# Kernel optimization log

Hardware: AMD Instinct MI355X
Metric: run time of the kernel (lower is better)

The kernel has to match this reference:

```python
import jax, jax.numpy as jnp
import numpy as np

H = 128      # num_hidden
HIN = 384    # num_in (h_E feature dim)
DFF = 512    # FFN inner dim = 4*H
SCALE = 30.0
EPS = 1e-5

def gelu(x):
    return jax.nn.gelu(x, approximate=False)

def linear(x, w, b):
    return x @ w.T + b

def layer_norm(x, w, b):
    mu = jnp.mean(x, axis=-1, keepdims=True)
    var = jnp.var(x, axis=-1, keepdims=True)
    return (x - mu) * jax.lax.rsqrt(var + EPS) * w + b


def setup_inputs() -> dict:
    key = jax.random.key(0)
    ks = jax.random.split(key, 10)
    B, N, K = 4, 2048, 48
    s = lambda d: 1.0 / np.sqrt(d)
    return {
        "h_V": jax.random.normal(ks[0], (B, N, H), jnp.float32),
        "h_E": jax.random.normal(ks[1], (B, N, K, HIN), jnp.float32),
        "mask_V": jnp.ones((B, N), jnp.float32),
        "mask_attend": jnp.ones((B, N, K), jnp.float32),
        "W1_w": jax.random.normal(ks[2], (H, H + HIN), jnp.float32) * s(H + HIN),
        "W1_b": jnp.zeros((H,), jnp.float32),
        "W2_w": jax.random.normal(ks[3], (H, H), jnp.float32) * s(H),
        "W2_b": jnp.zeros((H,), jnp.float32),
        "W3_w": jax.random.normal(ks[4], (H, H), jnp.float32) * s(H),
        "W3_b": jnp.zeros((H,), jnp.float32),
        "ln1_w": jnp.ones((H,), jnp.float32),
        "ln1_b": jnp.zeros((H,), jnp.float32),
        "Win_w": jax.random.normal(ks[5], (DFF, H), jnp.float32) * s(H),
        "Win_b": jnp.zeros((DFF,), jnp.float32),
        "Wout_w": jax.random.normal(ks[6], (H, DFF), jnp.float32) * s(DFF),
        "Wout_b": jnp.zeros((H,), jnp.float32),
        "ln2_w": jnp.ones((H,), jnp.float32),
        "ln2_b": jnp.zeros((H,), jnp.float32),
    }


def reference(h_V, h_E, mask_V, mask_attend,
              W1_w, W1_b, W2_w, W2_b, W3_w, W3_b,
              ln1_w, ln1_b, Win_w, Win_b, Wout_w, Wout_b, ln2_w, ln2_b):
    K = h_E.shape[-2]
    # broadcast node feats to neighbors and concat: [B, N, K, H+HIN]
    h_V_expand = jnp.broadcast_to(h_V[:, :, None, :], (*h_V.shape[:2], K, h_V.shape[-1]))
    h_EV = jnp.concatenate([h_V_expand, h_E], axis=-1)
    h_message = linear(gelu(linear(gelu(linear(h_EV, W1_w, W1_b)), W2_w, W2_b)), W3_w, W3_b)
    h_message = mask_attend[..., None] * h_message
    dh = jnp.sum(h_message, axis=-2) / SCALE
    h = layer_norm(h_V + dh, ln1_w, ln1_b)
    dh = linear(gelu(linear(h, Win_w, Win_b)), Wout_w, Wout_b)
    h = layer_norm(h + dh, ln2_w, ln2_b)
    return mask_V[..., None] * h
```

## Files before the change

kernel.cpp:

```cpp
#include <hip/hip_runtime.h>
#include <hip/hip_bf16.h>

#define H    128
#define HIN  384
#define FIN  512
#define KNB  48
#define DFF  512
#define NNODES 8192
#define NNB_F (KNB*HIN)

typedef float f32x4 __attribute__((ext_vector_type(4)));
typedef short bf16x8 __attribute__((ext_vector_type(8)));

__device__ __forceinline__ unsigned short f2bf(float x){
  union { float f; unsigned u; } v; v.f = x;
  unsigned r = v.u + 0x7FFFu + ((v.u >> 16) & 1u);
  return (unsigned short)(r >> 16);
}

__device__ __forceinline__ bf16x8 load8f_bf(const float* p){
  float4 a = *(const float4*)p;
  float4 b = *(const float4*)(p+4);
  bf16x8 o;
  o[0]=(short)f2bf(a.x); o[1]=(short)f2bf(a.y); o[2]=(short)f2bf(a.z); o[3]=(short)f2bf(a.w);
  o[4]=(short)f2bf(b.x); o[5]=(short)f2bf(b.y); o[6]=(short)f2bf(b.z); o[7]=(short)f2bf(b.w);
  return o;
}

__device__ __forceinline__ float gelu_f(float x){
  return 0.5f * x * (1.0f + erff(x * 0.70710678118654752f));
}

__device__ __forceinline__ f32x4 zero4(){ f32x4 z; z[0]=0.f;z[1]=0.f;z[2]=0.f;z[3]=0.f; return z; }

__global__ __launch_bounds__(256) void k_convert(
    const float* __restrict__ W1, const float* __restrict__ W2,
    const float* __restrict__ W3, const float* __restrict__ Win,
    const float* __restrict__ Wout, unsigned short* __restrict__ dst)
{
  int i0 = (blockIdx.x*256 + threadIdx.x)*4;
  #pragma unroll
  for (int t=0;t<4;t++){
    int idx = i0 + t;
    float v;
    if      (idx <  65536) v = W1[idx];
    else if (idx <  81920) v = W2[idx-65536];
    else if (idx <  98304) v = W3[idx-81920];
    else if (idx < 163840) v = Win[idx-98304];
    else                   v = Wout[idx-163840];
    dst[idx] = f2bf(v);
  }
}

__global__ __launch_bounds__(256) void k_bias1(
    const float* __restrict__ hV, const unsigned short* __restrict__ wW1,
    const float* __restrict__ W1b, float* __restrict__ bias1)
{
  int tid = threadIdx.x;
  int wid = tid>>6, lane = tid&63;
  int lr = lane&15, lg = lane>>4;
  int m0 = (blockIdx.x*4 + wid)*16;

  f32x4 acc[8];
  #pragma unroll
  for (int i=0;i<8;i++) acc[i] = zero4();

  #pragma unroll
  for (int ks=0; ks<4; ks++){
    bf16x8 a = load8f_bf(hV + (size_t)(m0+lr)*H + ks*32 + lg*8);
    #pragma unroll
    for (int nt=0; nt<8; nt++){
      bf16x8 b = *(const bf16x8*)(wW1 + (size_t)(nt*16+lr)*FIN + ks*32 + lg*8);
      acc[nt] = __builtin_amdgcn_mfma_f32_16x16x32_bf16(a, b, acc[nt], 0,0,0);
    }
  }
  #pragma unroll
  for (int nt=0; nt<8; nt++){
    int col = nt*16 + lr;
    float bv = W1b[col];
    #pragma unroll
    for (int e=0;e<4;e++){
      int row = lg*4 + e;
      bias1[(size_t)(m0+row)*H + col] = acc[nt][e] + bv;
    }
  }
}

__global__ __launch_bounds__(256) void k_message(
    const float* __restrict__ hV, const float* __restrict__ hE,
    const float* __restrict__ maskA,
    const unsigned short* __restrict__ wW1, const unsigned short* __restrict__ wW2,
    const unsigned short* __restrict__ wW3,
    const float* __restrict__ W2b, const float* __restrict__ W3b,
    const float* __restrict__ ln1w, const float* __restrict__ ln1b,
    const float* __restrict__ bias1, float* __restrict__ hmid)
{
  __shared__ __align__(16) unsigned short sA[48*392];
  __shared__ __align__(16) unsigned short sG1[48*136];
  __shared__ float sMask[48];
  __shared__ float sBias[128];
  __shared__ float sDh[128];

  int node = blockIdx.x;
  int tid  = threadIdx.x;
  const float* hEn = hE + (size_t)node * NNB_F;

  #pragma unroll
  for (int i=0;i<9;i++){
    int c = i*256 + tid;
    int row = c/48, cir = c - row*48;
    bf16x8 v = load8f_bf(hEn + (size_t)c*8);
    *(bf16x8*)(sA + row*392 + cir*8) = v;
  }
  if (tid < 48)  sMask[tid] = maskA[(size_t)node*KNB + tid];
  if (tid < 128) sBias[tid] = bias1[(size_t)node*H + tid];
  __syncthreads();

  int wid = tid>>6, lane = tid&63;
  int lr = lane&15, lg = lane>>4;

  f32x4 acc1[3][2];
  #pragma unroll
  for (int mt=0;mt<3;mt++){ acc1[mt][0]=zero4(); acc1[mt][1]=zero4(); }

  for (int ks=0; ks<12; ks++){
    bf16x8 a[3];
    #pragma unroll
    for (int mt=0;mt<3;mt++)
      a[mt] = *(const bf16x8*)(sA + (mt*16+lr)*392 + ks*32 + lg*8);
    #pragma unroll
    for (int j=0;j<2;j++){
      int nt = wid*2 + j;
      bf16x8 b = *(const bf16x8*)(wW1 + (size_t)(nt*16+lr)*FIN + (H + ks*32 + lg*8));
      #pragma unroll
      for (int mt=0;mt<3;mt++)
        acc1[mt][j] = __builtin_amdgcn_mfma_f32_16x16x32_bf16(a[mt], b, acc1[mt][j], 0,0,0);
    }
  }
  #pragma unroll
  for (int j=0;j<2;j++){
    int col = (wid*2+j)*16 + lr;
    float bv = sBias[col];
    #pragma unroll
    for (int mt=0;mt<3;mt++){
      #pragma unroll
      for (int e=0;e<4;e++){
        float g = gelu_f(acc1[mt][j][e] + bv);
        int row = mt*16 + lg*4 + e;
        sG1[row*136 + col] = f2bf(g);
      }
    }
  }
  __syncthreads();

  f32x4 acc2[3][2];
  #pragma unroll
  for (int mt=0;mt<3;mt++){ acc2[mt][0]=zero4(); acc2[mt][1]=zero4(); }
  #pragma unroll
  for (int ks=0; ks<4; ks++){
    bf16x8 a[3];
    #pragma unroll
    for (int mt=0;mt<3;mt++)
      a[mt] = *(const bf16x8*)(sG1 + (mt*16+lr)*136 + ks*32 + lg*8);
    #pragma unroll
    for (int j=0;j<2;j++){
      int nt = wid*2 + j;
      bf16x8 b = *(const bf16x8*)(wW2 + (size_t)(nt*16+lr)*H + ks*32 + lg*8);
      #pragma unroll
      for (int mt=0;mt<3;mt++)
        acc2[mt][j] = __builtin_amdgcn_mfma_f32_16x16x32_bf16(a[mt], b, acc2[mt][j], 0,0,0);
    }
  }
  unsigned short* sG2 = sA;
  #pragma unroll
  for (int j=0;j<2;j++){
    int col = (wid*2+j)*16 + lr;
    float bv = W2b[col];
    #pragma unroll
    for (int mt=0;mt<3;mt++){
      #pragma unroll
      for (int e=0;e<4;e++){
        float g = gelu_f(acc2[mt][j][e] + bv);
        int row = mt*16 + lg*4 + e;
        sG2[row*136 + col] = f2bf(g);
      }
    }
  }
  __syncthreads();

  f32x4 acc3[3][2];
  #pragma unroll
  for (int mt=0;mt<3;mt++){ acc3[mt][0]=zero4(); acc3[mt][1]=zero4(); }
  #pragma unroll
  for (int ks=0; ks<4; ks++){
    bf16x8 a[3];
    #pragma unroll
    for (int mt=0;mt<3;mt++)
      a[mt] = *(const bf16x8*)(sG2 + (mt*16+lr)*136 + ks*32 + lg*8);
    #pragma unroll
    for (int j=0;j<2;j++){
      int nt = wid*2 + j;
      bf16x8 b = *(const bf16x8*)(wW3 + (size_t)(nt*16+lr)*H + ks*32 + lg*8);
      #pragma unroll
      for (int mt=0;mt<3;mt++)
        acc3[mt][j] = __builtin_amdgcn_mfma_f32_16x16x32_bf16(a[mt], b, acc3[mt][j], 0,0,0);
    }
  }
  #pragma unroll
  for (int j=0;j<2;j++){
    int col = (wid*2+j)*16 + lr;
    float bv = W3b[col];
    float p = 0.f;
    #pragma unroll
    for (int mt=0;mt<3;mt++){
      #pragma unroll
      for (int e=0;e<4;e++){
        int row = mt*16 + lg*4 + e;
        p += (acc3[mt][j][e] + bv) * sMask[row];
      }
    }
    p += __shfl_xor(p, 16);
    p += __shfl_xor(p, 32);
    if (lane < 16) sDh[(wid*2+j)*16 + lane] = p;
  }
  __syncthreads();

  if (wid == 0){
    int c0 = lane, c1 = lane + 64;
    float t0 = hV[(size_t)node*H + c0] + sDh[c0]*(1.0f/30.0f);
    float t1 = hV[(size_t)node*H + c1] + sDh[c1]*(1.0f/30.0f);
    float s = t0 + t1, q = t0*t0 + t1*t1;
    #pragma unroll
    for (int off=1; off<64; off<<=1){ s += __shfl_xor(s, off); q += __shfl_xor(q, off); }
    float mu  = s * (1.0f/128.0f);
    float var = q * (1.0f/128.0f) - mu*mu;
    float rs  = rsqrtf(var + 1e-5f);
    hmid[(size_t)node*H + c0] = (t0-mu)*rs*ln1w[c0] + ln1b[c0];
    hmid[(size_t)node*H + c1] = (t1-mu)*rs*ln1w[c1] + ln1b[c1];
  }
}

__global__ __launch_bounds__(256) void k_ffn(
    const float* __restrict__ hmid, const unsigned short* __restrict__ wWin,
    const unsigned short* __restrict__ wWout,
    const float* __restrict__ Winb, const float* __restrict__ Woutb,
    const float* __restrict__ ln2w, const float* __restrict__ ln2b,
    const float* __restrict__ maskV, float* __restrict__ out)
{
  __shared__ __align__(16) unsigned short sH[32*136];
  __shared__ __align__(16) unsigned short sU[32*520];
  __shared__ float sT[32*132];

  int tid = threadIdx.x;
  int m0 = blockIdx.x * 32;

  #pragma unroll
  for (int i=0;i<2;i++){
    int c = i*256 + tid;
    int row = c>>4, cir = c&15;
    bf16x8 v = load8f_bf(hmid + (size_t)(m0+row)*H + cir*8);
    *(bf16x8*)(sH + row*136 + cir*8) = v;
  }
  __syncthreads();

  int wid = tid>>6, lane = tid&63;
  int lr = lane&15, lg = lane>>4;

  f32x4 acc[2][8];
  #pragma unroll
  for (int mt=0;mt<2;mt++)
    #pragma unroll
    for (int j=0;j<8;j++) acc[mt][j] = zero4();

  #pragma unroll
  for (int ks=0; ks<4; ks++){
    bf16x8 a[2];
    #pragma unroll
    for (int mt=0;mt<2;mt++)
      a[mt] = *(const bf16x8*)(sH + (mt*16+lr)*136 + ks*32 + lg*8);
    #pragma unroll
    for (int j=0;j<8;j++){
      int nt = wid*8 + j;
      bf16x8 b = *(const bf16x8*)(wWin + (size_t)(nt*16+lr)*H + ks*32 + lg*8);
      #pragma unroll
      for (int mt=0;mt<2;mt++)
        acc[mt][j] = __builtin_amdgcn_mfma_f32_16x16x32_bf16(a[mt], b, acc[mt][j], 0,0,0);
    }
  }
  #pragma unroll
  for (int j=0;j<8;j++){
    int col = (wid*8+j)*16 + lr;
    float bv = Winb[col];
    #pragma unroll
    for (int mt=0;mt<2;mt++){
      #pragma unroll
      for (int e=0;e<4;e++){
        float g = gelu_f(acc[mt][j][e] + bv);
        int row = mt*16 + lg*4 + e;
        sU[row*520 + col] = f2bf(g);
      }
    }
  }
  __syncthreads();

  f32x4 accO[2][2];
  #pragma unroll
  for (int mt=0;mt<2;mt++){ accO[mt][0]=zero4(); accO[mt][1]=zero4(); }

  for (int ks=0; ks<16; ks++){
    bf16x8 a[2];
    #pragma unroll
    for (int mt=0;mt<2;mt++)
      a[mt] = *(const bf16x8*)(sU + (mt*16+lr)*520 + ks*32 + lg*8);
    #pragma unroll
    for (int j=0;j<2;j++){
      int nt = wid*2 + j;
      bf16x8 b = *(const bf16x8*)(wWout + (size_t)(nt*16+lr)*DFF + ks*32 + lg*8);
      #pragma unroll
      for (int mt=0;mt<2;mt++)
        accO[mt][j] = __builtin_amdgcn_mfma_f32_16x16x32_bf16(a[mt], b, accO[mt][j], 0,0,0);
    }
  }
  #pragma unroll
  for (int j=0;j<2;j++){
    int col = (wid*2+j)*16 + lr;
    float bv = Woutb[col];
    #pragma unroll
    for (int mt=0;mt<2;mt++){
      #pragma unroll
      for (int e=0;e<4;e++){
        int row = mt*16 + lg*4 + e;
        float t = accO[mt][j][e] + bv + hmid[(size_t)(m0+row)*H + col];
        sT[row*132 + col] = t;
      }
    }
  }
  __syncthreads();

  int row = tid>>3, part = tid&7;
  float s=0.f, q=0.f;
  #pragma unroll
  for (int jj=0;jj<16;jj++){
    float v = sT[row*132 + part*16 + jj];
    s += v; q += v*v;
  }
  s += __shfl_xor(s,1); q += __shfl_xor(q,1);
  s += __shfl_xor(s,2); q += __shfl_xor(q,2);
  s += __shfl_xor(s,4); q += __shfl_xor(q,4);
  float mu  = s*(1.0f/128.0f);
  float var = q*(1.0f/128.0f) - mu*mu;
  float rs  = rsqrtf(var + 1e-5f);
  float mv  = maskV[m0+row];
  #pragma unroll
  for (int jj=0;jj<16;jj++){
    int c = part*16 + jj;
    out[(size_t)(m0+row)*H + c] = mv * ((sT[row*132+c]-mu)*rs*ln2w[c] + ln2b[c]);
  }
}

extern "C" void kernel_launch(void* const* d_in, const int* in_sizes, int n_in,
                              void* d_out, int out_size, void* d_ws, size_t ws_size,
                              hipStream_t stream)
{
  const float* hV    = (const float*)d_in[0];
  const float* hE    = (const float*)d_in[1];
  const float* maskV = (const float*)d_in[2];
  const float* maskA = (const float*)d_in[3];
  const float* W1w   = (const float*)d_in[4];
  const float* W1b   = (const float*)d_in[5];
  const float* W2w   = (const float*)d_in[6];
  const float* W2b   = (const float*)d_in[7];
  const float* W3w   = (const float*)d_in[8];
  const float* W3b   = (const float*)d_in[9];
  const float* ln1w  = (const float*)d_in[10];
  const float* ln1b  = (const float*)d_in[11];
  const float* Winw  = (const float*)d_in[12];
  const float* Winb  = (const float*)d_in[13];
  const float* Woutw = (const float*)d_in[14];
  const float* Woutb = (const float*)d_in[15];
  const float* ln2w  = (const float*)d_in[16];
  const float* ln2b  = (const float*)d_in[17];

  unsigned short* wAll  = (unsigned short*)d_ws;
  unsigned short* wW1   = wAll;
  unsigned short* wW2   = wAll + 65536;
  unsigned short* wW3   = wAll + 81920;
  unsigned short* wWin  = wAll + 98304;
  unsigned short* wWout = wAll + 163840;
  float* bias1 = (float*)((char*)d_ws + 458752);
  float* hmid  = (float*)d_out;
  float* outp  = (float*)d_out;

  k_convert<<<224, 256, 0, stream>>>(W1w, W2w, W3w, Winw, Woutw, wAll);
  k_bias1  <<<128, 256, 0, stream>>>(hV, wW1, W1b, bias1);
  k_message<<<NNODES, 256, 0, stream>>>(hV, hE, maskA, wW1, wW2, wW3,
                                        W2b, W3b, ln1w, ln1b, bias1, hmid);
  k_ffn    <<<NNODES/32, 256, 0, stream>>>(hmid, wWin, wWout, Winb, Woutb,
                                           ln2w, ln2b, maskV, outp);
}
```

Baseline: 285.4 us.

## Stream h_E directly from global into MFMA operands, shrink message-kernel LDS

The message kernel no longer stages the whole 48x384 h_E tile (about 37 KB) into shared memory. Each wave now loads its A fragments straight from global memory and converts them to bf16 in registers. A single small sG buffer is reused for both GELU intermediates, and launch bounds request 4 blocks per CU, so occupancy should rise and the staging pass plus one barrier disappear. In exchange, each of the four waves re-reads the same h_E rows from global/L2, with less coalesced 32-byte accesses. The float-to-bf16 conversion also switches to the library intrinsic.

```diff
diff --git a/kernel.cpp b/kernel.cpp
--- a/kernel.cpp
+++ b/kernel.cpp
@@ -12,18 +12,15 @@
 typedef float f32x4 __attribute__((ext_vector_type(4)));
 typedef short bf16x8 __attribute__((ext_vector_type(8)));
 
-__device__ __forceinline__ unsigned short f2bf(float x){
-  union { float f; unsigned u; } v; v.f = x;
-  unsigned r = v.u + 0x7FFFu + ((v.u >> 16) & 1u);
-  return (unsigned short)(r >> 16);
-}
-
-__device__ __forceinline__ bf16x8 load8f_bf(const float* p){
-  float4 a = *(const float4*)p;
-  float4 b = *(const float4*)(p+4);
+__device__ __forceinline__ short bfs(float x){
+  __hip_bfloat16 h = __float2bfloat16(x);
+  return *(short*)&h;
+}
+
+__device__ __forceinline__ bf16x8 pack8(float4 a, float4 b){
   bf16x8 o;
-  o[0]=(short)f2bf(a.x); o[1]=(short)f2bf(a.y); o[2]=(short)f2bf(a.z); o[3]=(short)f2bf(a.w);
-  o[4]=(short)f2bf(b.x); o[5]=(short)f2bf(b.y); o[6]=(short)f2bf(b.z); o[7]=(short)f2bf(b.w);
+  o[0]=bfs(a.x); o[1]=bfs(a.y); o[2]=bfs(a.z); o[3]=bfs(a.w);
+  o[4]=bfs(b.x); o[5]=bfs(b.y); o[6]=bfs(b.z); o[7]=bfs(b.w);
   return o;
 }
 
@@ -48,7 +45,7 @@
     else if (idx <  98304) v = W3[idx-81920];
     else if (idx < 163840) v = Win[idx-98304];
     else                   v = Wout[idx-163840];
-    dst[idx] = f2bf(v);
+    dst[idx] = (unsigned short)bfs(v);
   }
 }
 
@@ -67,7 +64,8 @@
 
   #pragma unroll
   for (int ks=0; ks<4; ks++){
-    bf16x8 a = load8f_bf(hV + (size_t)(m0+lr)*H + ks*32 + lg*8);
+    const float* p = hV + (size_t)(m0+lr)*H + ks*32 + lg*8;
+    bf16x8 a = pack8(*(const float4*)p, *(const float4*)(p+4));
     #pragma unroll
     for (int nt=0; nt<8; nt++){
       bf16x8 b = *(const bf16x8*)(wW1 + (size_t)(nt*16+lr)*FIN + ks*32 + lg*8);
@@ -86,7 +84,7 @@
   }
 }
 
-__global__ __launch_bounds__(256) void k_message(
+__global__ __launch_bounds__(256,4) void k_message(
     const float* __restrict__ hV, const float* __restrict__ hE,
     const float* __restrict__ maskA,
     const unsigned short* __restrict__ wW1, const unsigned short* __restrict__ wW2,
@@ -95,39 +93,33 @@
     const float* __restrict__ ln1w, const float* __restrict__ ln1b,
     const float* __restrict__ bias1, float* __restrict__ hmid)
 {
-  __shared__ __align__(16) unsigned short sA[48*392];
-  __shared__ __align__(16) unsigned short sG1[48*136];
+  __shared__ __align__(16) unsigned short sG[48*136];
   __shared__ float sMask[48];
   __shared__ float sBias[128];
   __shared__ float sDh[128];
 
   int node = blockIdx.x;
   int tid  = threadIdx.x;
-  const float* hEn = hE + (size_t)node * NNB_F;
-
-  #pragma unroll
-  for (int i=0;i<9;i++){
-    int c = i*256 + tid;
-    int row = c/48, cir = c - row*48;
-    bf16x8 v = load8f_bf(hEn + (size_t)c*8);
-    *(bf16x8*)(sA + row*392 + cir*8) = v;
-  }
   if (tid < 48)  sMask[tid] = maskA[(size_t)node*KNB + tid];
   if (tid < 128) sBias[tid] = bias1[(size_t)node*H + tid];
-  __syncthreads();
 
   int wid = tid>>6, lane = tid&63;
   int lr = lane&15, lg = lane>>4;
+  const float* hEn = hE + (size_t)node * NNB_F;
+  const float* aBase = hEn + (size_t)lr*HIN + lg*8;
 
   f32x4 acc1[3][2];
   #pragma unroll
   for (int mt=0;mt<3;mt++){ acc1[mt][0]=zero4(); acc1[mt][1]=zero4(); }
 
+  #pragma unroll 2
   for (int ks=0; ks<12; ks++){
     bf16x8 a[3];
     #pragma unroll
-    for (int mt=0;mt<3;mt++)
-      a[mt] = *(const bf16x8*)(sA + (mt*16+lr)*392 + ks*32 + lg*8);
+    for (int mt=0;mt<3;mt++){
+      const float* p = aBase + (size_t)mt*16*HIN + ks*32;
+      a[mt] = pack8(*(const float4*)p, *(const float4*)(p+4));
+    }
     #pragma unroll
     for (int j=0;j<2;j++){
       int nt = wid*2 + j;
@@ -137,6 +129,8 @@
         acc1[mt][j] = __builtin_amdgcn_mfma_f32_16x16x32_bf16(a[mt], b, acc1[mt][j], 0,0,0);
     }
   }
+  __syncthreads();
+
   #pragma unroll
   for (int j=0;j<2;j++){
     int col = (wid*2+j)*16 + lr;
@@ -147,7 +141,7 @@
       for (int e=0;e<4;e++){
         float g = gelu_f(acc1[mt][j][e] + bv);
         int row = mt*16 + lg*4 + e;
-        sG1[row*136 + col] = f2bf(g);
+        sG[row*136 + col] = (unsigned short)bfs(g);
       }
     }
   }
@@ -161,7 +155,7 @@
     bf16x8 a[3];
     #pragma unroll
     for (int mt=0;mt<3;mt++)
-      a[mt] = *(const bf16x8*)(sG1 + (mt*16+lr)*136 + ks*32 + lg*8);
+      a[mt] = *(const bf16x8*)(sG + (mt*16+lr)*136 + ks*32 + lg*8);
     #pragma unroll
     for (int j=0;j<2;j++){
       int nt = wid*2 + j;
@@ -171,7 +165,8 @@
         acc2[mt][j] = __builtin_amdgcn_mfma_f32_16x16x32_bf16(a[mt], b, acc2[mt][j], 0,0,0);
     }
   }
-  unsigned short* sG2 = sA;
+  __syncthreads();
+
   #pragma unroll
   for (int j=0;j<2;j++){
     int col = (wid*2+j)*16 + lr;
@@ -182,7 +177,7 @@
       for (int e=0;e<4;e++){
         float g = gelu_f(acc2[mt][j][e] + bv);
         int row = mt*16 + lg*4 + e;
-        sG2[row*136 + col] = f2bf(g);
+        sG[row*136 + col] = (unsigned short)bfs(g);
       }
     }
   }
@@ -196,7 +191,7 @@
     bf16x8 a[3];
     #pragma unroll
     for (int mt=0;mt<3;mt++)
-      a[mt] = *(const bf16x8*)(sG2 + (mt*16+lr)*136 + ks*32 + lg*8);
+      a[mt] = *(const bf16x8*)(sG + (mt*16+lr)*136 + ks*32 + lg*8);
     #pragma unroll
     for (int j=0;j<2;j++){
       int nt = wid*2 + j;
@@ -258,8 +253,8 @@
   for (int i=0;i<2;i++){
     int c = i*256 + tid;
     int row = c>>4, cir = c&15;
-    bf16x8 v = load8f_bf(hmid + (size_t)(m0+row)*H + cir*8);
-    *(bf16x8*)(sH + row*136 + cir*8) = v;
+    const float* p = hmid + (size_t)(m0+row)*H + cir*8;
+    *(bf16x8*)(sH + row*136 + cir*8) = pack8(*(const float4*)p, *(const float4*)(p+4));
   }
   __syncthreads();
 
@@ -297,7 +292,7 @@
       for (int e=0;e<4;e++){
         float g = gelu_f(acc[mt][j][e] + bv);
         int row = mt*16 + lg*4 + e;
-        sU[row*520 + col] = f2bf(g);
+        sU[row*520 + col] = (unsigned short)bfs(g);
       }
     }
   }
```

Result: slower. 454.0 us (+59.1%).
